# Kernel optimization log

Hardware: AMD Instinct MI355X
Metric: run time of the kernel (lower is better)

## Reference

```python
import jax, jax.numpy as jnp
import numpy as np

# Model dims (from ModelArgs defaults)
B, S, DIM = 1, 1024, 2880
H, HKV, HD = 64, 8, 64        # query heads, kv heads, head dim
GROUP = H // HKV              # 8 query heads per kv head
WINDOW = 128                  # sliding window (layer_idx=0 -> active)
THETA = 150000.0


def setup_inputs() -> dict:
    key = jax.random.key(0)
    ks = jax.random.split(key, 10)
    rn = lambda k, shape, sc: (jax.random.normal(k, shape, jnp.float32) * sc)
    return {
        "x": rn(ks[0], (B, S, DIM), 1.0),
        "wq_w": rn(ks[1], (H * HD, DIM), 0.02),
        "wq_b": rn(ks[2], (H * HD,), 0.02),
        "wk_w": rn(ks[3], (HKV * HD, DIM), 0.02),
        "wk_b": rn(ks[4], (HKV * HD,), 0.02),
        "wv_w": rn(ks[5], (HKV * HD, DIM), 0.02),
        "wv_b": rn(ks[6], (HKV * HD,), 0.02),
        "wo_w": rn(ks[7], (DIM, H * HD), 0.02),
        "wo_b": rn(ks[8], (DIM,), 0.02),
        "sinks": rn(ks[9], (H,), 1.0),
    }


def _rope(t):
    # t: [B, S, h, HD]; half-split (rotate_half) RoPE with base THETA
    half = HD // 2
    inv_freq = 1.0 / (THETA ** (jnp.arange(half, dtype=jnp.float32) * 2.0 / HD))
    ang = jnp.arange(S, dtype=jnp.float32)[:, None] * inv_freq      # [S, half]
    cos = jnp.cos(ang)[None, :, None, :]
    sin = jnp.sin(ang)[None, :, None, :]
    t1, t2 = t[..., :half], t[..., half:]
    return jnp.concatenate([t1 * cos - t2 * sin, t1 * sin + t2 * cos], axis=-1)


def reference(x, wq_w, wq_b, wk_w, wk_b, wv_w, wv_b, wo_w, wo_b, sinks):
    # Projections (nn.Linear: y = x @ W^T + b)
    q = (jnp.einsum('bsd,ed->bse', x, wq_w) + wq_b).reshape(B, S, H, HD)
    k = (jnp.einsum('bsd,ed->bse', x, wk_w) + wk_b).reshape(B, S, HKV, HD)
    v = (jnp.einsum('bsd,ed->bse', x, wv_w) + wv_b).reshape(B, S, HKV, HD)

    q = _rope(q)
    k = _rope(k)

    # GQA: expand kv heads to match query heads
    k = jnp.repeat(k, GROUP, axis=2)   # [B, S, H, HD]
    v = jnp.repeat(v, GROUP, axis=2)

    scale = HD ** -0.5
    scores = jnp.einsum('bihd,bjhd->bhij', q, k) * scale   # [B, H, S, S]

    # Causal + sliding-window mask: attend to j with 0 <= i-j < WINDOW
    i = jnp.arange(S)[:, None]
    j = jnp.arange(S)[None, :]
    allowed = (j <= i) & ((i - j) < WINDOW)
    scores = jnp.where(allowed, scores, jnp.float32(-1e30))

    # Softmax with per-head learnable sink logit folded into normalization
    sink = sinks[None, :, None, None]                       # [1, H, 1, 1]
    m = jnp.maximum(jnp.max(scores, axis=-1, keepdims=True), sink)
    e = jnp.exp(scores - m)
    denom = jnp.sum(e, axis=-1, keepdims=True) + jnp.exp(sink - m)
    probs = e / denom                                       # sink mass dropped

    out = jnp.einsum('bhij,bjhd->bihd', probs, v).reshape(B, S, H * HD)
    return jnp.einsum('bse,de->bsd', out, wo_w) + wo_b
```

## Files before the change

### kernel.cpp

```cpp
#include <hip/hip_runtime.h>

typedef __attribute__((ext_vector_type(4))) float f32x4;
typedef __attribute__((ext_vector_type(8))) short s16x8;
typedef unsigned short u16;

#define DEVI __device__ __forceinline__

DEVI u16 f2bf(float f) {
    union { float f; unsigned int u; } v; v.f = f;
    unsigned int r = v.u + 0x7FFFu + ((v.u >> 16) & 1u);
    return (u16)(r >> 16);
}
DEVI float bf2f(u16 b) {
    union { unsigned int u; float f; } v; v.u = ((unsigned int)b) << 16;
    return v.f;
}

typedef __attribute__((address_space(1))) void gv_t;
typedef __attribute__((address_space(3))) void sv_t;

#define GLOAD16(SRC, DST) __builtin_amdgcn_global_load_lds( \
    (gv_t*)(SRC), (sv_t*)(DST), 16, 0, 0)

DEVI f32x4 mfma_bf16(s16x8 a, s16x8 b, f32x4 c) {
    return __builtin_amdgcn_mfma_f32_16x16x32_bf16(a, b, c, 0, 0, 0);
}

__global__ void cvt_all_kernel(
    const float* __restrict__ x,  const float* __restrict__ wq, const float* __restrict__ wk,
    const float* __restrict__ wv, const float* __restrict__ wo,
    u16* __restrict__ xb, u16* __restrict__ wqb, u16* __restrict__ wkb,
    u16* __restrict__ wvb, u16* __restrict__ wob)
{
    int id = blockIdx.x * 256 + threadIdx.x;
    const float* s; u16* d; int off;
    if      (id < 737280)  { s = x;  d = xb;  off = id; }
    else if (id < 3686400) { s = wq; d = wqb; off = id - 737280; }
    else if (id < 4055040) { s = wk; d = wkb; off = id - 3686400; }
    else if (id < 4423680) { s = wv; d = wvb; off = id - 4055040; }
    else                   { s = wo; d = wob; off = id - 4423680; }
    f32x4 v = *(const f32x4*)(s + (size_t)off * 4);
    union { u16 u[4]; unsigned long long ll; } o;
    #pragma unroll
    for (int j = 0; j < 4; ++j) o.u[j] = f2bf(v[j]);
    *(unsigned long long*)(d + (size_t)off * 4) = o.ll;
}

__global__ __launch_bounds__(512, 2) void gemm256(
    const u16* __restrict__ A, int lda, int kit, int cpx,
    const u16* __restrict__ W0, int t0, int n0, int c0,
    const u16* __restrict__ W1, int t1, int n1, int c1,
    const u16* __restrict__ W2, int t2, int n2, int c2,
    u16* __restrict__ C, int ldc, long long cstride)
{
    __shared__ u16 Als[2][256 * 64];
    __shared__ u16 Bls[2][256 * 64];

    const int lin = blockIdx.x;
    const int ord = (lin & 7) * cpx + (lin >> 3);
    const int nbl = ord >> 2;
    const int yt  = ord & 3;

    const int tid  = threadIdx.x;
    const int lane = tid & 63;
    const int wid  = tid >> 6;
    const int li   = lane & 15;
    const int lg   = lane >> 4;
    const int m0   = yt * 256;

    const u16* W; int nt0, nsz, cb;
    if (nbl < t0)           { W = W0; nt0 = nbl * 256;             nsz = n0; cb = c0; }
    else if (nbl < t0 + t1) { W = W1; nt0 = (nbl - t0) * 256;      nsz = n1; cb = c1; }
    else                    { W = W2; nt0 = (nbl - t0 - t1) * 256; nsz = n2; cb = c2; }

    const int z  = blockIdx.z;
    const int S  = gridDim.z;
    const int it0 = (z * kit) / S;
    const int it1 = ((z + 1) * kit) / S;
    u16* Cp = C + (long long)z * cstride;

    const int wm = (wid >> 2) * 128;
    const int wn = (wid & 3) * 64;

    f32x4 acc[8][4];
    #pragma unroll
    for (int mi = 0; mi < 8; ++mi)
        #pragma unroll
        for (int ni = 0; ni < 4; ++ni)
            acc[mi][ni] = (f32x4){0.f, 0.f, 0.f, 0.f};

#define STAGE(BUF, IT)                                                          \
    do {                                                                        \
        int k0_ = (IT) * 64;                                                    \
        _Pragma("unroll")                                                       \
        for (int j = 0; j < 4; ++j) {                                           \
            int g_   = j * 512 + tid;                                           \
            int row_ = g_ >> 3;                                                 \
            int cs_  = (tid & 7) ^ (row_ & 7);                                  \
            const u16* sa_ = A + (size_t)(m0 + row_) * lda + k0_ + cs_ * 8;     \
            GLOAD16(sa_, &Als[BUF][g_ * 8]);                                    \
        }                                                                       \
        _Pragma("unroll")                                                       \
        for (int j = 0; j < 4; ++j) {                                           \
            int g_   = j * 512 + tid;                                           \
            int row_ = g_ >> 3;                                                 \
            int wr_  = nt0 + row_;                                              \
            if (wr_ > nsz - 1) wr_ = nsz - 1;               \
            int cs_  = (tid & 7) ^ (row_ & 7);                                  \
            const u16* sb_ = W + (size_t)wr_ * lda + k0_ + cs_ * 8;             \
            GLOAD16(sb_, &Bls[BUF][g_ * 8]);                                    \
        }                                                                       \
    } while (0)

    STAGE(0, it0);
    asm volatile("" ::: "memory");
    STAGE(1, it0 + 1);

    for (int it = it0; it < it1; ++it) {
        const int cur = (it - it0) & 1;

        if (it + 1 < it1) {
            asm volatile("s_waitcnt vmcnt(8)\n\ts_barrier" ::: "memory");
        } else {
            asm volatile("s_waitcnt vmcnt(0)\n\ts_barrier" ::: "memory");
        }

        s16x8 bfv[4][2];
        #pragma unroll
        for (int ni = 0; ni < 4; ++ni)
            #pragma unroll
            for (int kc = 0; kc < 2; ++kc) {
                int row = wn + ni * 16 + li;
                int ch  = (kc * 4 + lg) ^ (row & 7);
                bfv[ni][kc] = *(const s16x8*)&Bls[cur][row * 64 + ch * 8];
            }
        __builtin_amdgcn_s_setprio(1);
        #pragma unroll
        for (int mi = 0; mi < 8; ++mi) {
            s16x8 af[2];
            #pragma unroll
            for (int kc = 0; kc < 2; ++kc) {
                int row = wm + mi * 16 + li;
                int ch  = (kc * 4 + lg) ^ (row & 7);
                af[kc] = *(const s16x8*)&Als[cur][row * 64 + ch * 8];
            }
            #pragma unroll
            for (int ni = 0; ni < 4; ++ni)
                #pragma unroll
                for (int kc = 0; kc < 2; ++kc)
                    acc[mi][ni] = mfma_bf16(af[kc], bfv[ni][kc], acc[mi][ni]);
        }
        __builtin_amdgcn_s_setprio(0);

        asm volatile("s_waitcnt lgkmcnt(0)\n\ts_barrier" ::: "memory");

        if (it + 2 < it1) STAGE(cur, it + 2);
    }
#undef STAGE

    #pragma unroll
    for (int ni = 0; ni < 4; ++ni) {
        int colr = nt0 + wn + ni * 16 + li;
        if (colr < nsz) {
            #pragma unroll
            for (int mi = 0; mi < 8; ++mi)
                #pragma unroll
                for (int r = 0; r < 4; ++r) {
                    int row = m0 + wm + mi * 16 + lg * 4 + r;
                    Cp[(size_t)row * ldc + cb + colr] = f2bf(acc[mi][ni][r]);
                }
        }
    }
}

__global__ void rope_kernel(const u16* __restrict__ qkvp,
                            const float* __restrict__ qb, const float* __restrict__ kb,
                            const float* __restrict__ vb,
                            u16* __restrict__ qo, u16* __restrict__ ko, u16* __restrict__ vo)
{
    const long long PST = 1024LL * 5120;
    int id = blockIdx.x * 256 + threadIdx.x;
    int s  = id / 2560;
    int r  = id % 2560;
    const u16* r0 = qkvp + (size_t)s * 5120;
    if (r < 2304) {
        bool isq = r < 2048;
        int rr   = isq ? r : r - 2048;
        int hh   = rr >> 5;
        int d    = rr & 31;
        int col  = (isq ? 0 : 4096) + hh * 64 + d;
        int bcol = isq ? col : col - 4096;
        const float* bias = isq ? qb : kb;
        float t1 = bf2f(r0[col])      + bf2f(r0[col + PST])      + bf2f(r0[col + 2 * PST])      + bias[bcol];
        float t2 = bf2f(r0[col + 32]) + bf2f(r0[col + 32 + PST]) + bf2f(r0[col + 32 + 2 * PST]) + bias[bcol + 32];
        float ang = (float)s * exp2f((float)d * -0.5373314f);
        float sn, cs;
        sincosf(ang, &sn, &cs);
        float sc = isq ? 0.125f : 1.0f;
        float o1 = (t1 * cs - t2 * sn) * sc;
        float o2 = (t1 * sn + t2 * cs) * sc;
        u16* dst = isq ? qo : ko;
        int ldd  = isq ? 4096 : 512;
        dst[(size_t)s * ldd + bcol]      = f2bf(o1);
        dst[(size_t)s * ldd + bcol + 32] = f2bf(o2);
    } else {
        int e = (r - 2304) * 2;
        int c0 = 4608 + e;
        float v0 = bf2f(r0[c0])     + bf2f(r0[c0 + PST])     + bf2f(r0[c0 + 2 * PST])     + vb[e];
        float v1 = bf2f(r0[c0 + 1]) + bf2f(r0[c0 + 1 + PST]) + bf2f(r0[c0 + 1 + 2 * PST]) + vb[e + 1];
        vo[(size_t)s * 512 + e]     = f2bf(v0);
        vo[(size_t)s * 512 + e + 1] = f2bf(v1);
    }
}

__global__ void reduce_out_kernel(const u16* __restrict__ parts,
                                  const float* __restrict__ bias,
                                  float* __restrict__ out)
{
    int id = blockIdx.x * 256 + threadIdx.x;
    const long long stride = 1024LL * 2880;
    long long base = (long long)id * 8;
    float s[8];
    #pragma unroll
    for (int j = 0; j < 8; ++j) s[j] = 0.f;
    #pragma unroll
    for (int p = 0; p < 5; ++p) {
        s16x8 v = *(const s16x8*)(parts + p * stride + base);
        #pragma unroll
        for (int j = 0; j < 8; ++j) s[j] += bf2f((u16)v[j]);
    }
    int cb = (int)(base % 2880);
    f32x4 b0 = *(const f32x4*)(bias + cb);
    f32x4 b1 = *(const f32x4*)(bias + cb + 4);
    f32x4 o0 = {s[0] + b0[0], s[1] + b0[1], s[2] + b0[2], s[3] + b0[3]};
    f32x4 o1 = {s[4] + b1[0], s[5] + b1[1], s[6] + b1[2], s[7] + b1[3]};
    *(f32x4*)(out + base)     = o0;
    *(f32x4*)(out + base + 4) = o1;
}

__global__ __launch_bounds__(256, 2) void attn_kernel(
    const u16* __restrict__ Q, const u16* __restrict__ Kb, const u16* __restrict__ Vb,
    const float* __restrict__ sinks, u16* __restrict__ Ob)
{
    __shared__ u16 Kls[64 * 64];
    __shared__ u16 Pls[4][16 * 72];

    const int h    = blockIdx.x;
    const int qblk = blockIdx.y;
    const int kvh  = h >> 3;
    const int tid  = threadIdx.x;
    const int lane = tid & 63;
    const int w    = tid >> 6;
    const int li   = lane & 15;
    const int lg   = lane >> 4;
    const int qw   = qblk * 64 + w * 16;

    s16x8 aq[2];
    {
        const u16* qrow = Q + ((size_t)(qw + li) * 64 + h) * 64 + lg * 8;
        aq[0] = *(const s16x8*)(qrow);
        aq[1] = *(const s16x8*)(qrow + 32);
    }

    const float snk = sinks[h];
    float m_run[4], l_run[4];
    f32x4 oacc[4];
    #pragma unroll
    for (int r = 0; r < 4; ++r) { m_run[r] = snk; l_run[r] = 1.0f; }
    #pragma unroll
    for (int ni = 0; ni < 4; ++ni) oacc[ni] = (f32x4){0.f, 0.f, 0.f, 0.f};

    const int srow = tid >> 3;
    const int slc  = (tid & 7) ^ (srow & 7);

    for (int t = 0; t < 3; ++t) {
        int jt = qblk - 2 + t;
        if (jt < 0) continue;
        int j0 = jt * 64;

        #pragma unroll
        for (int it = 0; it < 2; ++it) {
            const u16* src = Kb + ((size_t)(j0 + it * 32 + srow) * 8 + kvh) * 64 + slc * 8;
            GLOAD16(src, &Kls[(it * 256 + w * 64) * 8]);
        }
        __syncthreads();

        f32x4 sc[4];
        #pragma unroll
        for (int nf = 0; nf < 4; ++nf) {
            sc[nf] = (f32x4){0.f, 0.f, 0.f, 0.f};
            #pragma unroll
            for (int kc = 0; kc < 2; ++kc) {
                int row = nf * 16 + li;
                int ch  = (kc * 4 + lg) ^ (row & 7);
                s16x8 bk = *(const s16x8*)&Kls[row * 64 + ch * 8];
                sc[nf] = mfma_bf16(aq[kc], bk, sc[nf]);
            }
        }

        #pragma unroll
        for (int r = 0; r < 4; ++r) {
            const int qg = qw + lg * 4 + r;
            float mx = -1e30f;
            #pragma unroll
            for (int nf = 0; nf < 4; ++nf) {
                int jg = j0 + nf * 16 + li;
                bool ok = (jg <= qg) && (qg - jg < 128);
                float v = ok ? sc[nf][r] : -1e30f;
                sc[nf][r] = v;
                mx = fmaxf(mx, v);
            }
            #pragma unroll
            for (int off = 1; off < 16; off <<= 1)
                mx = fmaxf(mx, __shfl_xor(mx, off));
            float mnew = fmaxf(m_run[r], mx);
            float corr = __expf(m_run[r] - mnew);
            m_run[r] = mnew;
            float rs = 0.f;
            #pragma unroll
            for (int nf = 0; nf < 4; ++nf) {
                float p = __expf(sc[nf][r] - mnew);
                rs += p;
                Pls[w][(lg * 4 + r) * 72 + nf * 16 + li] = f2bf(p);
            }
            #pragma unroll
            for (int off = 1; off < 16; off <<= 1)
                rs += __shfl_xor(rs, off);
            l_run[r] = l_run[r] * corr + rs;
            #pragma unroll
            for (int ni = 0; ni < 4; ++ni) oacc[ni][r] *= corr;
        }
        __syncthreads();

        #pragma unroll
        for (int kc = 0; kc < 2; ++kc) {
            s16x8 pa = *(const s16x8*)&Pls[w][li * 72 + kc * 32 + lg * 8];
            #pragma unroll
            for (int ni = 0; ni < 4; ++ni) {
                const u16* vsrc = Vb + ((size_t)(j0 + kc * 32 + lg * 8) * 8 + kvh) * 64 + ni * 16 + li;
                s16x8 bv;
                #pragma unroll
                for (int i = 0; i < 8; ++i) bv[i] = (short)vsrc[(size_t)i * 512];
                oacc[ni] = mfma_bf16(pa, bv, oacc[ni]);
            }
        }
    }

    #pragma unroll
    for (int r = 0; r < 4; ++r) {
        float inv = 1.0f / l_run[r];
        #pragma unroll
        for (int ni = 0; ni < 4; ++ni)
            Ob[((size_t)(qw + lg * 4 + r) * 64 + h) * 64 + ni * 16 + li] = f2bf(oacc[ni][r] * inv);
    }
}

extern "C" void kernel_launch(void* const* d_in, const int* in_sizes, int n_in,
                              void* d_out, int out_size, void* d_ws, size_t ws_size,
                              hipStream_t stream)
{
    const float* x     = (const float*)d_in[0];
    const float* wq_w  = (const float*)d_in[1];
    const float* wq_b  = (const float*)d_in[2];
    const float* wk_w  = (const float*)d_in[3];
    const float* wk_b  = (const float*)d_in[4];
    const float* wv_w  = (const float*)d_in[5];
    const float* wv_b  = (const float*)d_in[6];
    const float* wo_w  = (const float*)d_in[7];
    const float* wo_b  = (const float*)d_in[8];
    const float* sinks = (const float*)d_in[9];

    char* ws = (char*)d_ws;
    u16*   xb   = (u16*)(ws + 0);
    u16*   wqb  = (u16*)(ws + 5898240ULL);
    u16*   wkb  = (u16*)(ws + 29491200ULL);
    u16*   wvb  = (u16*)(ws + 32440320ULL);
    u16*   qkvp = (u16*)(ws + 35389440ULL);
    u16*   qr   = (u16*)(ws + 0);
    u16*   kr   = (u16*)(ws + 8388608ULL);
    u16*   vbf  = (u16*)(ws + 9437184ULL);
    u16*   attb = (u16*)(ws + 10485760ULL);
    u16*   oprt = (u16*)(ws + 58982400ULL);
    u16*   wob  = (u16*)(ws + 88473600ULL);

    (void)in_sizes; (void)n_in; (void)out_size; (void)ws_size;

    cvt_all_kernel<<<28800, 256, 0, stream>>>(x, wq_w, wk_w, wv_w, wo_w,
                                              xb, wqb, wkb, wvb, wob);
    gemm256<<<dim3(80, 1, 3), 512, 0, stream>>>(xb, 2880, 45, 10,
        wqb, 16, 4096, 0,
        wkb, 2, 512, 4096,
        wvb, 2, 512, 4608,
        qkvp, 5120, 1024LL * 5120);
    rope_kernel<<<10240, 256, 0, stream>>>(qkvp, wq_b, wk_b, wv_b, qr, kr, vbf);
    attn_kernel<<<dim3(64, 16), 256, 0, stream>>>(qr, kr, vbf, sinks, attb);
    gemm256<<<dim3(48, 1, 5), 512, 0, stream>>>(attb, 4096, 64, 6,
        wob, 12, 2880, 0,
        wob, 0, 0, 0,
        wob, 0, 0, 0,
        oprt, 2880, 1024LL * 2880);
    reduce_out_kernel<<<1440, 256, 0, stream>>>(oprt, wo_b, (float*)d_out);
}
```

Baseline: 141.5 us.

## Restructure GEMM main loop into 8-phase quadrant schedule with interleaved half-tile loads

Replaces the per-tile GEMM loop with an 8-phase schedule. Each phase computes one 128x128 quadrant of the 256x256 output tile and issues a half-tile global-to-LDS load for a future k-step, so memory transfers are spread across MFMA phases instead of issued in bulk. Warp ownership of outputs changes to 4 strided 64x32 quadrant pieces. It adds more barriers per k-step and more LDS fragment reloads per tile, and the vmcnt bookkeeping is fragile.

Result: no change. 139.0 us (-1.8%).

```diff
diff --git a/kernel.cpp b/kernel.cpp
--- a/kernel.cpp
+++ b/kernel.cpp
@@ -46,7 +46,7 @@
     *(unsigned long long*)(d + (size_t)off * 4) = o.ll;
 }
 
-__global__ __launch_bounds__(512, 2) void gemm256(
+__global__ __launch_bounds__(512, 2) void gemm8p(
     const u16* __restrict__ A, int lda, int kit, int cpx,
     const u16* __restrict__ W0, int t0, int n0, int c0,
     const u16* __restrict__ W1, int t1, int n1, int c1,
@@ -67,6 +67,8 @@
     const int li   = lane & 15;
     const int lg   = lane >> 4;
     const int m0   = yt * 256;
+    const int wr   = wid >> 2;
+    const int wc   = wid & 3;
 
     const u16* W; int nt0, nsz, cb;
     if (nbl < t0)           { W = W0; nt0 = nbl * 256;             nsz = n0; cb = c0; }
@@ -79,98 +81,125 @@
     const int it1 = ((z + 1) * kit) / S;
     u16* Cp = C + (long long)z * cstride;
 
-    const int wm = (wid >> 2) * 128;
-    const int wn = (wid & 3) * 64;
-
-    f32x4 acc[8][4];
-    #pragma unroll
-    for (int mi = 0; mi < 8; ++mi)
-        #pragma unroll
-        for (int ni = 0; ni < 4; ++ni)
-            acc[mi][ni] = (f32x4){0.f, 0.f, 0.f, 0.f};
-
-#define STAGE(BUF, IT)                                                          \
-    do {                                                                        \
-        int k0_ = (IT) * 64;                                                    \
-        _Pragma("unroll")                                                       \
-        for (int j = 0; j < 4; ++j) {                                           \
-            int g_   = j * 512 + tid;                                           \
-            int row_ = g_ >> 3;                                                 \
-            int cs_  = (tid & 7) ^ (row_ & 7);                                  \
-            const u16* sa_ = A + (size_t)(m0 + row_) * lda + k0_ + cs_ * 8;     \
-            GLOAD16(sa_, &Als[BUF][g_ * 8]);                                    \
-        }                                                                       \
-        _Pragma("unroll")                                                       \
-        for (int j = 0; j < 4; ++j) {                                           \
-            int g_   = j * 512 + tid;                                           \
-            int row_ = g_ >> 3;                                                 \
-            int wr_  = nt0 + row_;                                              \
-            if (wr_ > nsz - 1) wr_ = nsz - 1;               \
-            int cs_  = (tid & 7) ^ (row_ & 7);                                  \
-            const u16* sb_ = W + (size_t)wr_ * lda + k0_ + cs_ * 8;             \
-            GLOAD16(sb_, &Bls[BUF][g_ * 8]);                                    \
-        }                                                                       \
+    f32x4 acc[2][2][4][2];
+    #pragma unroll
+    for (int qm = 0; qm < 2; ++qm)
+        #pragma unroll
+        for (int qn = 0; qn < 2; ++qn)
+            #pragma unroll
+            for (int mi = 0; mi < 4; ++mi)
+                #pragma unroll
+                for (int ni = 0; ni < 2; ++ni)
+                    acc[qm][qn][mi][ni] = (f32x4){0.f, 0.f, 0.f, 0.f};
+
+    auto stage_half = [&](int isB, int tile, int h) {
+        if (tile >= it1) return;
+        const int k0 = tile * 64;
+        const int buf = tile & 1;
+        #pragma unroll
+        for (int j = 0; j < 2; ++j) {
+            int g  = j * 512 + tid;
+            int lr = g >> 3;
+            int c8 = g & 7;
+            int row = h * 128 + lr;
+            int sc  = c8 ^ (lr & 7);
+            if (isB) {
+                int wrow = nt0 + row; if (wrow > nsz - 1) wrow = nsz - 1;
+                GLOAD16(W + (size_t)wrow * lda + k0 + sc * 8,
+                        &Bls[buf][row * 64 + c8 * 8]);
+            } else {
+                GLOAD16(A + (size_t)(m0 + row) * lda + k0 + sc * 8,
+                        &Als[buf][row * 64 + c8 * 8]);
+            }
+        }
+    };
+
+#define PHASE(TILE, QM, QN, SISB, STILE, SH, VM)                               \
+    do {                                                                       \
+        const int buf_ = (TILE) & 1;                                           \
+        s16x8 af_[4][2], bf_[2][2];                                            \
+        _Pragma("unroll")                                                      \
+        for (int mi = 0; mi < 4; ++mi)                                         \
+            _Pragma("unroll")                                                  \
+            for (int kc = 0; kc < 2; ++kc) {                                   \
+                int row = (QM) * 128 + wr * 64 + mi * 16 + li;                 \
+                int ch  = (kc * 4 + lg) ^ (row & 7);                           \
+                af_[mi][kc] = *(const s16x8*)&Als[buf_][row * 64 + ch * 8];    \
+            }                                                                  \
+        _Pragma("unroll")                                                      \
+        for (int ni = 0; ni < 2; ++ni)                                         \
+            _Pragma("unroll")                                                  \
+            for (int kc = 0; kc < 2; ++kc) {                                   \
+                int row = (QN) * 128 + wc * 32 + ni * 16 + li;                 \
+                int ch  = (kc * 4 + lg) ^ (row & 7);                           \
+                bf_[ni][kc] = *(const s16x8*)&Bls[buf_][row * 64 + ch * 8];    \
+            }                                                                  \
+        stage_half((SISB), (STILE), (SH));                                     \
+        {                                                                      \
+            int vm_ = (VM);                                                    \
+            if (vm_ == 4)      asm volatile("s_waitcnt vmcnt(4)" ::: "memory");\
+            else if (vm_ == 0) asm volatile("s_waitcnt vmcnt(0)" ::: "memory");\
+        }                                                                      \
+        asm volatile("s_barrier" ::: "memory");                                \
+        __builtin_amdgcn_s_setprio(1);                                         \
+        _Pragma("unroll")                                                      \
+        for (int mi = 0; mi < 4; ++mi)                                         \
+            _Pragma("unroll")                                                  \
+            for (int ni = 0; ni < 2; ++ni)                                     \
+                _Pragma("unroll")                                              \
+                for (int kc = 0; kc < 2; ++kc)                                 \
+                    acc[QM][QN][mi][ni] =                                      \
+                        mfma_bf16(af_[mi][kc], bf_[ni][kc], acc[QM][QN][mi][ni]); \
+        __builtin_amdgcn_s_setprio(0);                                         \
+        asm volatile("s_barrier" ::: "memory");                                \
     } while (0)
 
-    STAGE(0, it0);
-    asm volatile("" ::: "memory");
-    STAGE(1, it0 + 1);
-
-    for (int it = it0; it < it1; ++it) {
-        const int cur = (it - it0) & 1;
-
-        if (it + 1 < it1) {
-            asm volatile("s_waitcnt vmcnt(8)\n\ts_barrier" ::: "memory");
-        } else {
-            asm volatile("s_waitcnt vmcnt(0)\n\ts_barrier" ::: "memory");
-        }
-
-        s16x8 bfv[4][2];
-        #pragma unroll
-        for (int ni = 0; ni < 4; ++ni)
-            #pragma unroll
-            for (int kc = 0; kc < 2; ++kc) {
-                int row = wn + ni * 16 + li;
-                int ch  = (kc * 4 + lg) ^ (row & 7);
-                bfv[ni][kc] = *(const s16x8*)&Bls[cur][row * 64 + ch * 8];
-            }
-        __builtin_amdgcn_s_setprio(1);
-        #pragma unroll
-        for (int mi = 0; mi < 8; ++mi) {
-            s16x8 af[2];
-            #pragma unroll
-            for (int kc = 0; kc < 2; ++kc) {
-                int row = wm + mi * 16 + li;
-                int ch  = (kc * 4 + lg) ^ (row & 7);
-                af[kc] = *(const s16x8*)&Als[cur][row * 64 + ch * 8];
-            }
-            #pragma unroll
-            for (int ni = 0; ni < 4; ++ni)
+    stage_half(0, it0, 0);
+    stage_half(1, it0, 0);
+    stage_half(0, it0, 1);
+    stage_half(1, it0, 1);
+    stage_half(0, it0 + 1, 0);
+    stage_half(1, it0 + 1, 0);
+    asm volatile("s_waitcnt vmcnt(4)" ::: "memory");
+    asm volatile("s_barrier" ::: "memory");
+
+    int t = it0;
+    for (; t + 1 < it1; t += 2) {
+        PHASE(t,     0, 0, 0, t + 1, 1, -1);
+        PHASE(t,     0, 1, 1, t + 1, 1, -1);
+        PHASE(t,     1, 0, 0, t + 2, 0, -1);
+        PHASE(t,     1, 1, 1, t + 2, 0, (t + 2 < it1) ? 4 : 0);
+        PHASE(t + 1, 0, 0, 0, t + 2, 1, -1);
+        PHASE(t + 1, 0, 1, 1, t + 2, 1, -1);
+        PHASE(t + 1, 1, 0, 0, t + 3, 0, -1);
+        PHASE(t + 1, 1, 1, 1, t + 3, 0, 4);
+    }
+    if (t < it1) {
+        PHASE(t, 0, 0, 0, it1, 0, 0);
+        PHASE(t, 0, 1, 0, it1, 0, -1);
+        PHASE(t, 1, 0, 0, it1, 0, -1);
+        PHASE(t, 1, 1, 0, it1, 0, -1);
+    }
+#undef PHASE
+
+    #pragma unroll
+    for (int qn = 0; qn < 2; ++qn)
+        #pragma unroll
+        for (int ni = 0; ni < 2; ++ni) {
+            int colr = nt0 + qn * 128 + wc * 32 + ni * 16 + li;
+            if (colr < nsz) {
                 #pragma unroll
-                for (int kc = 0; kc < 2; ++kc)
-                    acc[mi][ni] = mfma_bf16(af[kc], bfv[ni][kc], acc[mi][ni]);
-        }
-        __builtin_amdgcn_s_setprio(0);
-
-        asm volatile("s_waitcnt lgkmcnt(0)\n\ts_barrier" ::: "memory");
-
-        if (it + 2 < it1) STAGE(cur, it + 2);
-    }
-#undef STAGE
-
-    #pragma unroll
-    for (int ni = 0; ni < 4; ++ni) {
-        int colr = nt0 + wn + ni * 16 + li;
-        if (colr < nsz) {
-            #pragma unroll
-            for (int mi = 0; mi < 8; ++mi)
-                #pragma unroll
-                for (int r = 0; r < 4; ++r) {
-                    int row = m0 + wm + mi * 16 + lg * 4 + r;
-                    Cp[(size_t)row * ldc + cb + colr] = f2bf(acc[mi][ni][r]);
-                }
-        }
-    }
+                for (int qm = 0; qm < 2; ++qm)
+                    #pragma unroll
+                    for (int mi = 0; mi < 4; ++mi)
+                        #pragma unroll
+                        for (int r = 0; r < 4; ++r) {
+                            int row = m0 + qm * 128 + wr * 64 + mi * 16 + lg * 4 + r;
+                            Cp[(size_t)row * ldc + cb + colr] =
+                                f2bf(acc[qm][qn][mi][ni][r]);
+                        }
+            }
+        }
 }
 
 __global__ void rope_kernel(const u16* __restrict__ qkvp,
@@ -387,14 +416,14 @@
 
     cvt_all_kernel<<<28800, 256, 0, stream>>>(x, wq_w, wk_w, wv_w, wo_w,
                                               xb, wqb, wkb, wvb, wob);
-    gemm256<<<dim3(80, 1, 3), 512, 0, stream>>>(xb, 2880, 45, 10,
+    gemm8p<<<dim3(80, 1, 3), 512, 0, stream>>>(xb, 2880, 45, 10,
         wqb, 16, 4096, 0,
         wkb, 2, 512, 4096,
         wvb, 2, 512, 4608,
         qkvp, 5120, 1024LL * 5120);
     rope_kernel<<<10240, 256, 0, stream>>>(qkvp, wq_b, wk_b, wv_b, qr, kr, vbf);
     attn_kernel<<<dim3(64, 16), 256, 0, stream>>>(qr, kr, vbf, sinks, attb);
-    gemm256<<<dim3(48, 1, 5), 512, 0, stream>>>(attb, 4096, 64, 6,
+    gemm8p<<<dim3(48, 1, 5), 512, 0, stream>>>(attb, 4096, 64, 6,
         wob, 12, 2880, 0,
         wob, 0, 0, 0,
         wob, 0, 0, 0,
```
